# Performance work log

Measured on AMD Instinct MI355X. Metric: run time of the kernel, lower is better.

The kernel has to match this reference:

```python
import jax, jax.numpy as jnp
import numpy as np
import math

EPS = 1.0
N_IT = 10

def _sinkhorn_plan(C, eps, n_it):
    # C: [N, S, Sk] cost matrix; uniform marginals; log-domain Sinkhorn.
    n_rows, n_cols = C.shape[-2], C.shape[-1]
    log_mu = jnp.full(C.shape[:-1], -math.log(n_rows), C.dtype)
    log_nu = jnp.full(C.shape[:-2] + (n_cols,), -math.log(n_cols), C.dtype)

    def M(u, v):
        return (-C + u[..., :, None] + v[..., None, :]) / eps

    def body(carry, _):
        u, v = carry
        u = eps * (log_mu - jax.scipy.special.logsumexp(M(u, v), axis=-1)) + u
        v = eps * (log_nu - jax.scipy.special.logsumexp(M(u, v), axis=-2)) + v
        return (u, v), None

    u0 = jnp.zeros(C.shape[:-1], C.dtype)
    v0 = jnp.zeros(C.shape[:-2] + (C.shape[-1],), C.dtype)
    (u, v), _ = jax.lax.scan(body, (u0, v0), None, length=n_it)
    return jnp.exp(M(u, v))  # transport plan pi


def setup_inputs() -> dict:
    key = jax.random.key(0)
    kq, kk, kv = jax.random.split(key, 3)
    B, H, S, D = 2, 8, 1024, 64
    scale = 0.1  # keep exp(QK^T) numerically safe, as the model would via trained weights
    query = jax.random.normal(kq, (B, H, S, D), jnp.float32) * scale
    k_ = jax.random.normal(kk, (B, H, S, D), jnp.float32) * scale
    value = jax.random.normal(kv, (B, H, S, D), jnp.float32)
    return {"query": query, "key": k_, "value": value}


def reference(query, key, value):
    d = query.shape[-1]
    # exp-score attention (note: exp of raw QK^T, then divide by sqrt(d))
    scores = jnp.exp(jnp.einsum('bhqd,bhkd->bhqk', query, key)) / math.sqrt(d)
    B, H, S, Sk = scores.shape
    attn = scores.reshape(B * H, S, Sk)
    pi = _sinkhorn_plan(attn, EPS, N_IT)
    p_attn = (pi * Sk).reshape(B, H, S, Sk)  # row-stochastic doubly-normalized attention
    out = jnp.einsum('bhqk,bhkd->bhqd', p_attn, value)
    return out, p_attn
```

## Files before the change

kernel.cpp:

```cpp
#include <hip/hip_runtime.h>
#include <math.h>

#define NH   16
#define SEQ  1024
#define DIM  64
#define MUV  (1.0f/1024.0f)
#define KSTRIDE 2048

typedef __attribute__((ext_vector_type(8))) short bf16x8;
typedef __attribute__((ext_vector_type(4))) float f32x4;

__device__ __forceinline__ float frcp(float x){ return __builtin_amdgcn_rcpf(x); }
__device__ __forceinline__ float bf2f(unsigned short u){
  union { unsigned int i; float f; } v; v.i = ((unsigned int)u) << 16; return v.f;
}
__device__ __forceinline__ unsigned short f2bf(float f){
  union { float f; unsigned int i; } v; v.f = f;
  return (unsigned short)((v.i + 0x7FFFu + ((v.i >> 16) & 1u)) >> 16);
}

__global__ __launch_bounds__(256) void qk_kernel(const float* __restrict__ Q,
                                                 const float* __restrict__ Kin,
                                                 unsigned short* __restrict__ Kb) {
  __shared__ unsigned short QS[64 * 64];
  __shared__ unsigned short ST[64 * 64];
  __shared__ unsigned short Ob[64 * 64];
  const int h  = blockIdx.y;
  const int r0 = blockIdx.x * 64;
  const int t  = threadIdx.x;
  const int lane = t & 63, w = t >> 6, fr = lane & 15, fq = lane >> 4;
  const float* Qg = Q   + ((size_t)h * SEQ + r0) * DIM;
  const float* Kg = Kin + (size_t)h * SEQ * DIM;

  {
    const int r = t >> 4, c4 = (t & 15) * 4;
#pragma unroll
    for (int q = 0; q < 4; q++){
      const int row = r + 16 * q;
      const float4 v = *(const float4*)(Qg + row * DIM + c4);
      ushort4 u4 = make_ushort4(f2bf(v.x), f2bf(v.y), f2bf(v.z), f2bf(v.w));
      *(ushort4*)((char*)QS + row * 128 + ((c4 * 2) ^ ((row & 7) << 4))) = u4;
    }
  }
  __syncthreads();

  const int qrow = w * 16 + fr;
  const bf16x8 qa0 = *(const bf16x8*)((char*)QS + qrow * 128 + ((fq * 16)      ^ ((qrow & 7) << 4)));
  const bf16x8 qa1 = *(const bf16x8*)((char*)QS + qrow * 128 + ((64 + fq * 16) ^ ((qrow & 7) << 4)));

  for (int cc = 0; cc < 16; cc++){
    __syncthreads();
    {
      const int r = t >> 4, c4 = (t & 15) * 4;
      const float* g = Kg + (size_t)cc * 64 * DIM;
#pragma unroll
      for (int q = 0; q < 4; q++){
        const int row = r + 16 * q;
        const float4 v = *(const float4*)(g + row * DIM + c4);
        ushort4 u4 = make_ushort4(f2bf(v.x), f2bf(v.y), f2bf(v.z), f2bf(v.w));
        *(ushort4*)((char*)ST + row * 128 + ((c4 * 2) ^ ((row & 7) << 4))) = u4;
      }
    }
    __syncthreads();
#pragma unroll
    for (int ct = 0; ct < 4; ct++){
      const int krow = ct * 16 + fr;
      const bf16x8 kb0 = *(const bf16x8*)((char*)ST + krow * 128 + ((fq * 16)      ^ ((krow & 7) << 4)));
      const bf16x8 kb1 = *(const bf16x8*)((char*)ST + krow * 128 + ((64 + fq * 16) ^ ((krow & 7) << 4)));
      f32x4 acc = {0.f, 0.f, 0.f, 0.f};
      acc = __builtin_amdgcn_mfma_f32_16x16x32_bf16(qa0, kb0, acc, 0, 0, 0);
      acc = __builtin_amdgcn_mfma_f32_16x16x32_bf16(qa1, kb1, acc, 0, 0, 0);
#pragma unroll
      for (int r = 0; r < 4; r++){
        const int roww = w * 16 + fq * 4 + r;
        const float kv = __expf(-__expf(acc[r]) * 0.125f);
        Ob[roww * 64 + ct * 16 + fr] = f2bf(kv);
      }
    }
    __syncthreads();
    {
      const int row = t >> 2, c16 = (t & 3) * 16;
      unsigned short* dst = Kb + (size_t)(h * SEQ + r0 + row) * KSTRIDE + cc * 64 + c16;
      *(uint4*)dst       = *(const uint4*)&Ob[row * 64 + c16];
      *(uint4*)(dst + 8) = *(const uint4*)&Ob[row * 64 + c16 + 8];
    }
  }
}

__global__ __launch_bounds__(256, 2) void sink_iter(const unsigned short* __restrict__ Kb,
                                                    const float* __restrict__ cprev,
                                                    float* __restrict__ cnext,
                                                    float* __restrict__ avg,
                                                    int first) {
  __shared__ unsigned short Ksh[32 * 1024];
  __shared__ float bsh[1024];
  __shared__ float ash[32];
  const int h = blockIdx.y, ch = blockIdx.x, r0 = ch * 32, t = threadIdx.x;

  if (first){
    *(float4*)&bsh[t * 4] = make_float4(1.f, 1.f, 1.f, 1.f);
  } else {
    float4 s = make_float4(0, 0, 0, 0);
    const float* cp = cprev + (size_t)h * 32 * 1024 + t * 4;
#pragma unroll 8
    for (int sl = 0; sl < 32; sl++){
      const float4 v = *(const float4*)(cp + (size_t)sl * 1024);
      s.x += v.x; s.y += v.y; s.z += v.z; s.w += v.w;
    }
    *(float4*)&bsh[t * 4] = make_float4(MUV * frcp(s.x), MUV * frcp(s.y),
                                        MUV * frcp(s.z), MUV * frcp(s.w));
  }
  __syncthreads();

  const int row = t >> 3, off8 = t & 7;
  const unsigned short* gk = Kb + (size_t)(h * SEQ + r0 + row) * KSTRIDE;
  float acc = 0.f;
#pragma unroll
  for (int p = 0; p < 16; p++){
    const int idx = (p * 8 + off8) * 8;
    const uint4 g = *(const uint4*)(gk + idx);
    *(uint4*)&Ksh[row * 1024 + idx] = g;
    const float4 b0 = *(const float4*)&bsh[idx];
    const float4 b1 = *(const float4*)&bsh[idx + 4];
    acc += bf2f((unsigned short)(g.x)) * b0.x + bf2f((unsigned short)(g.x >> 16)) * b0.y
         + bf2f((unsigned short)(g.y)) * b0.z + bf2f((unsigned short)(g.y >> 16)) * b0.w
         + bf2f((unsigned short)(g.z)) * b1.x + bf2f((unsigned short)(g.z >> 16)) * b1.y
         + bf2f((unsigned short)(g.w)) * b1.z + bf2f((unsigned short)(g.w >> 16)) * b1.w;
  }
#pragma unroll
  for (int m = 1; m < 8; m <<= 1) acc += __shfl_xor(acc, m);
  if (off8 == 0){
    const float a = MUV * frcp(acc);
    ash[row] = a;
    avg[h * SEQ + r0 + row] = a;
  }
  __syncthreads();

  float4 ca = make_float4(0, 0, 0, 0);
#pragma unroll 8
  for (int i = 0; i < 32; i++){
    const ushort4 k4 = *(const ushort4*)&Ksh[i * 1024 + t * 4];
    const float a = ash[i];
    ca.x += bf2f(k4.x) * a; ca.y += bf2f(k4.y) * a;
    ca.z += bf2f(k4.z) * a; ca.w += bf2f(k4.w) * a;
  }
  *(float4*)(cnext + ((size_t)h * 32 + ch) * 1024 + t * 4) = ca;
}

__global__ __launch_bounds__(256, 2) void pv_kernel(const unsigned short* __restrict__ Kb,
                                                    const float* __restrict__ V,
                                                    const float* __restrict__ cpart,
                                                    const float* __restrict__ avg,
                                                    float* __restrict__ out) {
  __shared__ unsigned short Ksh[16 * 1024];
  __shared__ unsigned short Vsh[256 * 64];
  __shared__ float bsh[1024];
  __shared__ float ash[16];
  const int h = blockIdx.y, ch = blockIdx.x, r0 = ch * 16, t = threadIdx.x;
  const int lane = t & 63, w = t >> 6, fr = lane & 15, fq = lane >> 4;

  {
    float4 s = make_float4(0, 0, 0, 0);
    const float* cp = cpart + (size_t)h * 32 * 1024 + t * 4;
#pragma unroll 8
    for (int sl = 0; sl < 32; sl++){
      const float4 v = *(const float4*)(cp + (size_t)sl * 1024);
      s.x += v.x; s.y += v.y; s.z += v.z; s.w += v.w;
    }
    *(float4*)&bsh[t * 4] = make_float4(MUV * frcp(s.x), MUV * frcp(s.y),
                                        MUV * frcp(s.z), MUV * frcp(s.w));
  }
  if (t < 16) ash[t] = 1024.f * avg[h * SEQ + r0 + t];

  {
#pragma unroll
    for (int s = 0; s < 8; s++){
      const int u = s * 256 + t;
      const int row = u >> 7, uo = u & 127;
      const unsigned short* src = Kb + (size_t)(h * SEQ + r0 + row) * KSTRIDE + uo * 8;
      *(uint4*)((char*)Ksh + row * 2048 + ((uo * 16) ^ ((row & 7) << 4))) = *(const uint4*)src;
    }
  }
  __syncthreads();

  const float ascale = ash[fr];
  f32x4 oacc = {0.f, 0.f, 0.f, 0.f};
  const float* Vg = V + (size_t)h * SEQ * DIM;

  for (int vq = 0; vq < 4; vq++){
    __syncthreads();
    {
#pragma unroll
      for (int p = 0; p < 4; p++){
        const int j = p * 64 + (t >> 2);
        const int piece = t & 3;
        const float* g = Vg + (size_t)(vq * 256 + j) * DIM + piece * 16;
        union { unsigned short u[16]; uint4 q[2]; } pk;
#pragma unroll
        for (int k = 0; k < 4; k++){
          const float4 v = *(const float4*)(g + k * 4);
          pk.u[k*4+0] = f2bf(v.x); pk.u[k*4+1] = f2bf(v.y);
          pk.u[k*4+2] = f2bf(v.z); pk.u[k*4+3] = f2bf(v.w);
        }
        const int sw = (j & 7) << 4;
        *(uint4*)((char*)Vsh + j * 128 + (((piece * 32)      ) ^ sw)) = pk.q[0];
        *(uint4*)((char*)Vsh + j * 128 + (((piece * 32) + 16 ) ^ sw)) = pk.q[1];
      }
    }
    __syncthreads();
#pragma unroll
    for (int vc = 0; vc < 4; vc++){
#pragma unroll
      for (int half = 0; half < 2; half++){
        const int jl = vc * 64 + half * 32;
        const int jg = vq * 256 + jl;
        const int k0 = jg + fq * 8;
        const bf16x8 kx8 = *(const bf16x8*)((char*)Ksh + fr * 2048 + ((k0 * 2) ^ ((fr & 7) << 4)));
        const float4 b0 = *(const float4*)&bsh[k0];
        const float4 b1 = *(const float4*)&bsh[k0 + 4];
        const float bv[8] = {b0.x, b0.y, b0.z, b0.w, b1.x, b1.y, b1.z, b1.w};
        union { unsigned short u[8]; bf16x8 v; } pa;
#pragma unroll
        for (int e = 0; e < 8; e++)
          pa.u[e] = f2bf(ascale * bv[e] * bf2f((unsigned short)kx8[e]));
        union { unsigned int wv[4]; bf16x8 v; } vb;
        const int dcol = (w * 16 + fr) * 2;
#pragma unroll
        for (int e2 = 0; e2 < 4; e2++){
          const int j0 = jl + fq * 8 + e2 * 2;
          const unsigned int lo = *(const unsigned short*)((char*)Vsh + j0 * 128 + (dcol ^ ((j0 & 7) << 4)));
          const unsigned int hi = *(const unsigned short*)((char*)Vsh + (j0 + 1) * 128 + (dcol ^ (((j0 + 1) & 7) << 4)));
          vb.wv[e2] = lo | (hi << 16);
        }
        oacc = __builtin_amdgcn_mfma_f32_16x16x32_bf16(pa.v, vb.v, oacc, 0, 0, 0);
      }
    }
  }

  float* og = out + ((size_t)h * SEQ + r0) * DIM + w * 16 + fr;
#pragma unroll
  for (int r = 0; r < 4; r++)
    og[(size_t)(fq * 4 + r) * DIM] = oacc[r];
}

__global__ __launch_bounds__(256, 2) void pwrite_kernel(const unsigned short* __restrict__ Kb,
                                                        float* __restrict__ Pmat,
                                                        const float* __restrict__ cpart,
                                                        const float* __restrict__ avg) {
  __shared__ unsigned short Ksh[32 * 1024];
  __shared__ float bsh[1024];
  __shared__ float ash[32];
  const int h = blockIdx.y, ch = blockIdx.x, r0 = ch * 32, t = threadIdx.x;

  {
    float4 s = make_float4(0, 0, 0, 0);
    const float* cp = cpart + (size_t)h * 32 * 1024 + t * 4;
#pragma unroll 8
    for (int sl = 0; sl < 32; sl++){
      const float4 v = *(const float4*)(cp + (size_t)sl * 1024);
      s.x += v.x; s.y += v.y; s.z += v.z; s.w += v.w;
    }
    *(float4*)&bsh[t * 4] = make_float4(MUV * frcp(s.x), MUV * frcp(s.y),
                                        MUV * frcp(s.z), MUV * frcp(s.w));
  }
  if (t < 32) ash[t] = 1024.f * avg[h * SEQ + r0 + t];

  const int row = t >> 3, off8 = t & 7;
  const unsigned short* gk = Kb + (size_t)(h * SEQ + r0 + row) * KSTRIDE;
#pragma unroll
  for (int p = 0; p < 16; p++){
    const int idx = (p * 8 + off8) * 8;
    *(uint4*)&Ksh[row * 1024 + idx] = *(const uint4*)(gk + idx);
  }
  __syncthreads();

  const float ar = ash[row];
  float* prow = Pmat + (size_t)(h * SEQ + r0 + row) * SEQ;
#pragma unroll
  for (int p = 0; p < 16; p++){
    const int idx = (p * 8 + off8) * 8;
    const uint4 g = *(const uint4*)&Ksh[row * 1024 + idx];
    const float4 b0 = *(const float4*)&bsh[idx];
    const float4 b1 = *(const float4*)&bsh[idx + 4];
    float4 o0, o1;
    o0.x = ar * b0.x * bf2f((unsigned short)(g.x));
    o0.y = ar * b0.y * bf2f((unsigned short)(g.x >> 16));
    o0.z = ar * b0.z * bf2f((unsigned short)(g.y));
    o0.w = ar * b0.w * bf2f((unsigned short)(g.y >> 16));
    o1.x = ar * b1.x * bf2f((unsigned short)(g.z));
    o1.y = ar * b1.y * bf2f((unsigned short)(g.z >> 16));
    o1.z = ar * b1.z * bf2f((unsigned short)(g.w));
    o1.w = ar * b1.w * bf2f((unsigned short)(g.w >> 16));
    *(float4*)(prow + idx)     = o0;
    *(float4*)(prow + idx + 4) = o1;
  }
}

extern "C" void kernel_launch(void* const* d_in, const int* in_sizes, int n_in,
                              void* d_out, int out_size, void* d_ws, size_t ws_size,
                              hipStream_t stream) {
  (void)in_sizes; (void)n_in; (void)out_size; (void)ws_size;
  const float* Q   = (const float*)d_in[0];
  const float* Kin = (const float*)d_in[1];
  const float* V   = (const float*)d_in[2];
  float* out  = (float*)d_out;
  float* Pmat = out + (size_t)NH * SEQ * DIM;
  unsigned short* Kb = (unsigned short*)Pmat;

  float* ws  = (float*)d_ws;
  float* cp0 = ws;
  float* cp1 = ws + (size_t)NH * 32 * SEQ;
  float* avg = ws + (size_t)2 * NH * 32 * SEQ;

  qk_kernel<<<dim3(16, 16), 256, 0, stream>>>(Q, Kin, Kb);
  for (int it = 0; it < 10; it++){
    const float* cprev = (it & 1) ? cp0 : cp1;
    float*       cnext = (it & 1) ? cp1 : cp0;
    sink_iter<<<dim3(32, 16), 256, 0, stream>>>(Kb, cprev, cnext, avg, it == 0 ? 1 : 0);
  }
  pv_kernel<<<dim3(64, 16), 256, 0, stream>>>(Kb, V, cp1, avg, out);
  pwrite_kernel<<<dim3(32, 16), 256, 0, stream>>>(Kb, Pmat, cp1, avg);
}
```

Before: 274.9 us.

## Recompute Gibbs kernel via MFMA each Sinkhorn iteration instead of storing it

Stops materialising the bf16 kernel matrix exp(-exp(QK)/8) in global memory. Each Sinkhorn iteration now recomputes QK^T with MFMA from bf16 Q/K copies held in the workspace. A new prep kernel converts Q, K and a transposed V to bf16 once. The P-matrix write and the PV product are fused into one final kernel. This swaps about 32MB of kernel-matrix traffic per iteration for extra matrix-core work and two exponentials per element per iteration.

```diff
diff --git a/kernel.cpp b/kernel.cpp
--- a/kernel.cpp
+++ b/kernel.cpp
@@ -5,7 +5,6 @@
 #define SEQ  1024
 #define DIM  64
 #define MUV  (1.0f/1024.0f)
-#define KSTRIDE 2048
 
 typedef __attribute__((ext_vector_type(8))) short bf16x8;
 typedef __attribute__((ext_vector_type(4))) float f32x4;
@@ -19,83 +18,65 @@
   return (unsigned short)((v.i + 0x7FFFu + ((v.i >> 16) & 1u)) >> 16);
 }
 
-__global__ __launch_bounds__(256) void qk_kernel(const float* __restrict__ Q,
-                                                 const float* __restrict__ Kin,
-                                                 unsigned short* __restrict__ Kb) {
-  __shared__ unsigned short QS[64 * 64];
-  __shared__ unsigned short ST[64 * 64];
-  __shared__ unsigned short Ob[64 * 64];
-  const int h  = blockIdx.y;
-  const int r0 = blockIdx.x * 64;
-  const int t  = threadIdx.x;
-  const int lane = t & 63, w = t >> 6, fr = lane & 15, fq = lane >> 4;
-  const float* Qg = Q   + ((size_t)h * SEQ + r0) * DIM;
-  const float* Kg = Kin + (size_t)h * SEQ * DIM;
-
-  {
-    const int r = t >> 4, c4 = (t & 15) * 4;
-#pragma unroll
-    for (int q = 0; q < 4; q++){
-      const int row = r + 16 * q;
-      const float4 v = *(const float4*)(Qg + row * DIM + c4);
-      ushort4 u4 = make_ushort4(f2bf(v.x), f2bf(v.y), f2bf(v.z), f2bf(v.w));
-      *(ushort4*)((char*)QS + row * 128 + ((c4 * 2) ^ ((row & 7) << 4))) = u4;
-    }
-  }
-  __syncthreads();
-
-  const int qrow = w * 16 + fr;
-  const bf16x8 qa0 = *(const bf16x8*)((char*)QS + qrow * 128 + ((fq * 16)      ^ ((qrow & 7) << 4)));
-  const bf16x8 qa1 = *(const bf16x8*)((char*)QS + qrow * 128 + ((64 + fq * 16) ^ ((qrow & 7) << 4)));
-
-  for (int cc = 0; cc < 16; cc++){
+__global__ __launch_bounds__(256) void prep_kernel(const float* __restrict__ Q,
+                                                   const float* __restrict__ K,
+                                                   const float* __restrict__ V,
+                                                   unsigned short* __restrict__ Qbf,
+                                                   unsigned short* __restrict__ Kbf,
+                                                   unsigned short* __restrict__ Vt) {
+  __shared__ float Vsh[64][68];
+  const int h = blockIdx.y, ck = blockIdx.x, t = threadIdx.x;
+  const int r = t >> 2, cp = (t & 3) * 16;
+  const size_t gbase = ((size_t)h * SEQ + ck * 64 + r) * DIM + cp;
+  {
+    union { unsigned short u[16]; uint4 q[2]; } pk;
+#pragma unroll
+    for (int k = 0; k < 4; k++){
+      const float4 v = *(const float4*)(Q + gbase + k * 4);
+      pk.u[k*4+0]=f2bf(v.x); pk.u[k*4+1]=f2bf(v.y); pk.u[k*4+2]=f2bf(v.z); pk.u[k*4+3]=f2bf(v.w);
+    }
+    *(uint4*)(Qbf + gbase) = pk.q[0];
+    *(uint4*)(Qbf + gbase + 8) = pk.q[1];
+  }
+  {
+    union { unsigned short u[16]; uint4 q[2]; } pk;
+#pragma unroll
+    for (int k = 0; k < 4; k++){
+      const float4 v = *(const float4*)(K + gbase + k * 4);
+      pk.u[k*4+0]=f2bf(v.x); pk.u[k*4+1]=f2bf(v.y); pk.u[k*4+2]=f2bf(v.z); pk.u[k*4+3]=f2bf(v.w);
+    }
+    *(uint4*)(Kbf + gbase) = pk.q[0];
+    *(uint4*)(Kbf + gbase + 8) = pk.q[1];
+  }
+  {
+#pragma unroll
+    for (int k = 0; k < 4; k++)
+      *(float4*)&Vsh[r][cp + k * 4] = *(const float4*)(V + gbase + k * 4);
     __syncthreads();
-    {
-      const int r = t >> 4, c4 = (t & 15) * 4;
-      const float* g = Kg + (size_t)cc * 64 * DIM;
-#pragma unroll
-      for (int q = 0; q < 4; q++){
-        const int row = r + 16 * q;
-        const float4 v = *(const float4*)(g + row * DIM + c4);
-        ushort4 u4 = make_ushort4(f2bf(v.x), f2bf(v.y), f2bf(v.z), f2bf(v.w));
-        *(ushort4*)((char*)ST + row * 128 + ((c4 * 2) ^ ((row & 7) << 4))) = u4;
-      }
-    }
-    __syncthreads();
-#pragma unroll
-    for (int ct = 0; ct < 4; ct++){
-      const int krow = ct * 16 + fr;
-      const bf16x8 kb0 = *(const bf16x8*)((char*)ST + krow * 128 + ((fq * 16)      ^ ((krow & 7) << 4)));
-      const bf16x8 kb1 = *(const bf16x8*)((char*)ST + krow * 128 + ((64 + fq * 16) ^ ((krow & 7) << 4)));
-      f32x4 acc = {0.f, 0.f, 0.f, 0.f};
-      acc = __builtin_amdgcn_mfma_f32_16x16x32_bf16(qa0, kb0, acc, 0, 0, 0);
-      acc = __builtin_amdgcn_mfma_f32_16x16x32_bf16(qa1, kb1, acc, 0, 0, 0);
-#pragma unroll
-      for (int r = 0; r < 4; r++){
-        const int roww = w * 16 + fq * 4 + r;
-        const float kv = __expf(-__expf(acc[r]) * 0.125f);
-        Ob[roww * 64 + ct * 16 + fr] = f2bf(kv);
-      }
-    }
-    __syncthreads();
-    {
-      const int row = t >> 2, c16 = (t & 3) * 16;
-      unsigned short* dst = Kb + (size_t)(h * SEQ + r0 + row) * KSTRIDE + cc * 64 + c16;
-      *(uint4*)dst       = *(const uint4*)&Ob[row * 64 + c16];
-      *(uint4*)(dst + 8) = *(const uint4*)&Ob[row * 64 + c16 + 8];
-    }
-  }
-}
-
-__global__ __launch_bounds__(256, 2) void sink_iter(const unsigned short* __restrict__ Kb,
-                                                    const float* __restrict__ cprev,
-                                                    float* __restrict__ cnext,
-                                                    float* __restrict__ avg,
-                                                    int first) {
+    const int dd = t >> 2, jp = (t & 3) * 16;
+    union { unsigned short u[16]; uint4 q[2]; } pk;
+#pragma unroll
+    for (int k = 0; k < 16; k++) pk.u[k] = f2bf(Vsh[jp + k][dd]);
+    unsigned short* dst = Vt + ((size_t)h * DIM + dd) * SEQ + ck * 64 + jp;
+    *(uint4*)dst       = pk.q[0];
+    *(uint4*)(dst + 8) = pk.q[1];
+  }
+}
+
+__global__ __launch_bounds__(256, 2)
+void sink_rc(const unsigned short* __restrict__ Qbf,
+             const unsigned short* __restrict__ Kbf,
+             const float* __restrict__ cprev,
+             float* __restrict__ cnext,
+             float* __restrict__ avg,
+             int first)
+{
   __shared__ unsigned short Ksh[32 * 1024];
   __shared__ float bsh[1024];
+  __shared__ float rsum[4][32];
   __shared__ float ash[32];
   const int h = blockIdx.y, ch = blockIdx.x, r0 = ch * 32, t = threadIdx.x;
+  const int lane = t & 63, w = t >> 6, fr = lane & 15, fq = lane >> 4;
 
   if (first){
     *(float4*)&bsh[t * 4] = make_float4(1.f, 1.f, 1.f, 1.f);
@@ -112,34 +93,68 @@
   }
   __syncthreads();
 
-  const int row = t >> 3, off8 = t & 7;
-  const unsigned short* gk = Kb + (size_t)(h * SEQ + r0 + row) * KSTRIDE;
-  float acc = 0.f;
-#pragma unroll
-  for (int p = 0; p < 16; p++){
-    const int idx = (p * 8 + off8) * 8;
-    const uint4 g = *(const uint4*)(gk + idx);
-    *(uint4*)&Ksh[row * 1024 + idx] = g;
-    const float4 b0 = *(const float4*)&bsh[idx];
-    const float4 b1 = *(const float4*)&bsh[idx + 4];
-    acc += bf2f((unsigned short)(g.x)) * b0.x + bf2f((unsigned short)(g.x >> 16)) * b0.y
-         + bf2f((unsigned short)(g.y)) * b0.z + bf2f((unsigned short)(g.y >> 16)) * b0.w
-         + bf2f((unsigned short)(g.z)) * b1.x + bf2f((unsigned short)(g.z >> 16)) * b1.y
-         + bf2f((unsigned short)(g.w)) * b1.z + bf2f((unsigned short)(g.w >> 16)) * b1.w;
-  }
-#pragma unroll
-  for (int m = 1; m < 8; m <<= 1) acc += __shfl_xor(acc, m);
-  if (off8 == 0){
-    const float a = MUV * frcp(acc);
-    ash[row] = a;
-    avg[h * SEQ + r0 + row] = a;
+  const unsigned short* qp = Qbf + ((size_t)h * SEQ + r0 + fr) * DIM + fq * 8;
+  const bf16x8 qa00 = *(const bf16x8*)qp;
+  const bf16x8 qa01 = *(const bf16x8*)(qp + 32);
+  const bf16x8 qa10 = *(const bf16x8*)(qp + 16 * DIM);
+  const bf16x8 qa11 = *(const bf16x8*)(qp + 16 * DIM + 32);
+
+  float rp[8] = {0.f,0.f,0.f,0.f,0.f,0.f,0.f,0.f};
+
+#pragma unroll 2
+  for (int cc = 0; cc < 16; cc++){
+    const int c0 = cc * 64 + w * 16;
+    const unsigned short* kp = Kbf + ((size_t)h * SEQ + c0 + fr) * DIM + fq * 8;
+    const bf16x8 kb0 = *(const bf16x8*)kp;
+    const bf16x8 kb1 = *(const bf16x8*)(kp + 32);
+    f32x4 a0 = {0.f,0.f,0.f,0.f}, a1 = {0.f,0.f,0.f,0.f};
+    a0 = __builtin_amdgcn_mfma_f32_16x16x32_bf16(qa00, kb0, a0, 0, 0, 0);
+    a0 = __builtin_amdgcn_mfma_f32_16x16x32_bf16(qa01, kb1, a0, 0, 0, 0);
+    a1 = __builtin_amdgcn_mfma_f32_16x16x32_bf16(qa10, kb0, a1, 0, 0, 0);
+    a1 = __builtin_amdgcn_mfma_f32_16x16x32_bf16(qa11, kb1, a1, 0, 0, 0);
+    const float bcol = bsh[c0 + fr];
+    const int col2 = (c0 + fr) * 2;
+#pragma unroll
+    for (int r = 0; r < 4; r++){
+      const int row0 = fq * 4 + r;
+      const float kv0 = __expf(-0.125f * __expf(a0[r]));
+      const unsigned short ku0 = f2bf(kv0);
+      *(unsigned short*)((char*)Ksh + row0 * 2048 + (col2 ^ ((row0 & 7) << 4))) = ku0;
+      rp[r] += bf2f(ku0) * bcol;
+      const int row1 = 16 + fq * 4 + r;
+      const float kv1 = __expf(-0.125f * __expf(a1[r]));
+      const unsigned short ku1 = f2bf(kv1);
+      *(unsigned short*)((char*)Ksh + row1 * 2048 + (col2 ^ ((row1 & 7) << 4))) = ku1;
+      rp[4 + r] += bf2f(ku1) * bcol;
+    }
+  }
+
+#pragma unroll
+  for (int m = 1; m <= 8; m <<= 1){
+#pragma unroll
+    for (int i = 0; i < 8; i++) rp[i] += __shfl_xor(rp[i], m);
+  }
+  if (fr == 0){
+#pragma unroll
+    for (int r = 0; r < 4; r++){
+      rsum[w][fq * 4 + r]      = rp[r];
+      rsum[w][16 + fq * 4 + r] = rp[4 + r];
+    }
   }
   __syncthreads();
+  if (t < 32){
+    const float rs = rsum[0][t] + rsum[1][t] + rsum[2][t] + rsum[3][t];
+    const float a = MUV * frcp(rs);
+    ash[t] = a;
+    avg[h * SEQ + r0 + t] = a;
+  }
+  __syncthreads();
 
   float4 ca = make_float4(0, 0, 0, 0);
+  const int bo = t * 8;
 #pragma unroll 8
   for (int i = 0; i < 32; i++){
-    const ushort4 k4 = *(const ushort4*)&Ksh[i * 1024 + t * 4];
+    const ushort4 k4 = *(const ushort4*)((char*)Ksh + i * 2048 + (bo ^ ((i & 7) << 4)));
     const float a = ash[i];
     ca.x += bf2f(k4.x) * a; ca.y += bf2f(k4.y) * a;
     ca.z += bf2f(k4.z) * a; ca.w += bf2f(k4.w) * a;
@@ -147,16 +162,19 @@
   *(float4*)(cnext + ((size_t)h * 32 + ch) * 1024 + t * 4) = ca;
 }
 
-__global__ __launch_bounds__(256, 2) void pv_kernel(const unsigned short* __restrict__ Kb,
-                                                    const float* __restrict__ V,
-                                                    const float* __restrict__ cpart,
-                                                    const float* __restrict__ avg,
-                                                    float* __restrict__ out) {
-  __shared__ unsigned short Ksh[16 * 1024];
-  __shared__ unsigned short Vsh[256 * 64];
+__global__ __launch_bounds__(256, 2)
+void final_rc(const unsigned short* __restrict__ Qbf,
+              const unsigned short* __restrict__ Kbf,
+              const unsigned short* __restrict__ Vt,
+              const float* __restrict__ cpart,
+              const float* __restrict__ avg,
+              float* __restrict__ Pmat,
+              float* __restrict__ out)
+{
+  __shared__ unsigned short Ksh[32 * 1024];
   __shared__ float bsh[1024];
-  __shared__ float ash[16];
-  const int h = blockIdx.y, ch = blockIdx.x, r0 = ch * 16, t = threadIdx.x;
+  __shared__ float ash[32];
+  const int h = blockIdx.y, ch = blockIdx.x, r0 = ch * 32, t = threadIdx.x;
   const int lane = t & 63, w = t >> 6, fr = lane & 15, fq = lane >> 4;
 
   {
@@ -170,154 +188,121 @@
     *(float4*)&bsh[t * 4] = make_float4(MUV * frcp(s.x), MUV * frcp(s.y),
                                         MUV * frcp(s.z), MUV * frcp(s.w));
   }
-  if (t < 16) ash[t] = 1024.f * avg[h * SEQ + r0 + t];
-
-  {
-#pragma unroll
-    for (int s = 0; s < 8; s++){
-      const int u = s * 256 + t;
-      const int row = u >> 7, uo = u & 127;
-      const unsigned short* src = Kb + (size_t)(h * SEQ + r0 + row) * KSTRIDE + uo * 8;
-      *(uint4*)((char*)Ksh + row * 2048 + ((uo * 16) ^ ((row & 7) << 4))) = *(const uint4*)src;
+  if (t < 32) ash[t] = 1024.f * avg[h * SEQ + r0 + t];
+
+  const unsigned short* qp = Qbf + ((size_t)h * SEQ + r0 + fr) * DIM + fq * 8;
+  const bf16x8 qa00 = *(const bf16x8*)qp;
+  const bf16x8 qa01 = *(const bf16x8*)(qp + 32);
+  const bf16x8 qa10 = *(const bf16x8*)(qp + 16 * DIM);
+  const bf16x8 qa11 = *(const bf16x8*)(qp + 16 * DIM + 32);
+
+#pragma unroll 2
+  for (int cc = 0; cc < 16; cc++){
+    const int c0 = cc * 64 + w * 16;
+    const unsigned short* kp = Kbf + ((size_t)h * SEQ + c0 + fr) * DIM + fq * 8;
+    const bf16x8 kb0 = *(const bf16x8*)kp;
+    const bf16x8 kb1 = *(const bf16x8*)(kp + 32);
+    f32x4 a0 = {0.f,0.f,0.f,0.f}, a1 = {0.f,0.f,0.f,0.f};
+    a0 = __builtin_amdgcn_mfma_f32_16x16x32_bf16(qa00, kb0, a0, 0, 0, 0);
+    a0 = __builtin_amdgcn_mfma_f32_16x16x32_bf16(qa01, kb1, a0, 0, 0, 0);
+    a1 = __builtin_amdgcn_mfma_f32_16x16x32_bf16(qa10, kb0, a1, 0, 0, 0);
+    a1 = __builtin_amdgcn_mfma_f32_16x16x32_bf16(qa11, kb1, a1, 0, 0, 0);
+    const int col2 = (c0 + fr) * 2;
+#pragma unroll
+    for (int r = 0; r < 4; r++){
+      const int row0 = fq * 4 + r;
+      *(unsigned short*)((char*)Ksh + row0 * 2048 + (col2 ^ ((row0 & 7) << 4))) =
+          f2bf(__expf(-0.125f * __expf(a0[r])));
+      const int row1 = 16 + fq * 4 + r;
+      *(unsigned short*)((char*)Ksh + row1 * 2048 + (col2 ^ ((row1 & 7) << 4))) =
+          f2bf(__expf(-0.125f * __expf(a1[r])));
     }
   }
   __syncthreads();
 
-  const float ascale = ash[fr];
-  f32x4 oacc = {0.f, 0.f, 0.f, 0.f};
-  const float* Vg = V + (size_t)h * SEQ * DIM;
-
-  for (int vq = 0; vq < 4; vq++){
-    __syncthreads();
-    {
-#pragma unroll
-      for (int p = 0; p < 4; p++){
-        const int j = p * 64 + (t >> 2);
-        const int piece = t & 3;
-        const float* g = Vg + (size_t)(vq * 256 + j) * DIM + piece * 16;
-        union { unsigned short u[16]; uint4 q[2]; } pk;
-#pragma unroll
-        for (int k = 0; k < 4; k++){
-          const float4 v = *(const float4*)(g + k * 4);
-          pk.u[k*4+0] = f2bf(v.x); pk.u[k*4+1] = f2bf(v.y);
-          pk.u[k*4+2] = f2bf(v.z); pk.u[k*4+3] = f2bf(v.w);
-        }
-        const int sw = (j & 7) << 4;
-        *(uint4*)((char*)Vsh + j * 128 + (((piece * 32)      ) ^ sw)) = pk.q[0];
-        *(uint4*)((char*)Vsh + j * 128 + (((piece * 32) + 16 ) ^ sw)) = pk.q[1];
-      }
-    }
-    __syncthreads();
-#pragma unroll
-    for (int vc = 0; vc < 4; vc++){
-#pragma unroll
-      for (int half = 0; half < 2; half++){
-        const int jl = vc * 64 + half * 32;
-        const int jg = vq * 256 + jl;
-        const int k0 = jg + fq * 8;
-        const bf16x8 kx8 = *(const bf16x8*)((char*)Ksh + fr * 2048 + ((k0 * 2) ^ ((fr & 7) << 4)));
-        const float4 b0 = *(const float4*)&bsh[k0];
-        const float4 b1 = *(const float4*)&bsh[k0 + 4];
-        const float bv[8] = {b0.x, b0.y, b0.z, b0.w, b1.x, b1.y, b1.z, b1.w};
-        union { unsigned short u[8]; bf16x8 v; } pa;
-#pragma unroll
-        for (int e = 0; e < 8; e++)
-          pa.u[e] = f2bf(ascale * bv[e] * bf2f((unsigned short)kx8[e]));
-        union { unsigned int wv[4]; bf16x8 v; } vb;
-        const int dcol = (w * 16 + fr) * 2;
-#pragma unroll
-        for (int e2 = 0; e2 < 4; e2++){
-          const int j0 = jl + fq * 8 + e2 * 2;
-          const unsigned int lo = *(const unsigned short*)((char*)Vsh + j0 * 128 + (dcol ^ ((j0 & 7) << 4)));
-          const unsigned int hi = *(const unsigned short*)((char*)Vsh + (j0 + 1) * 128 + (dcol ^ (((j0 + 1) & 7) << 4)));
-          vb.wv[e2] = lo | (hi << 16);
-        }
-        oacc = __builtin_amdgcn_mfma_f32_16x16x32_bf16(pa.v, vb.v, oacc, 0, 0, 0);
-      }
-    }
+  {
+    const int prow = t >> 3, pc = t & 7;
+    const float ar = ash[prow];
+    const int swp = (prow & 7) << 4;
+    float* pg = Pmat + ((size_t)h * SEQ + r0 + prow) * SEQ;
+#pragma unroll
+    for (int p16 = 0; p16 < 16; p16++){
+      const int colb = (p16 * 8 + pc) * 8;
+      const uint4 kq = *(const uint4*)((char*)Ksh + prow * 2048 + ((colb * 2) ^ swp));
+      const float4 b0 = *(const float4*)&bsh[colb];
+      const float4 b1 = *(const float4*)&bsh[colb + 4];
+      float4 o0, o1;
+      o0.x = ar * b0.x * bf2f((unsigned short)(kq.x));
+      o0.y = ar * b0.y * bf2f((unsigned short)(kq.x >> 16));
+      o0.z = ar * b0.z * bf2f((unsigned short)(kq.y));
+      o0.w = ar * b0.w * bf2f((unsigned short)(kq.y >> 16));
+      o1.x = ar * b1.x * bf2f((unsigned short)(kq.z));
+      o1.y = ar * b1.y * bf2f((unsigned short)(kq.z >> 16));
+      o1.z = ar * b1.z * bf2f((unsigned short)(kq.w));
+      o1.w = ar * b1.w * bf2f((unsigned short)(kq.w >> 16));
+      *(float4*)(pg + colb)     = o0;
+      *(float4*)(pg + colb + 4) = o1;
+    }
+  }
+
+  f32x4 o0 = {0.f,0.f,0.f,0.f}, o1 = {0.f,0.f,0.f,0.f};
+  const float ar0 = ash[fr];
+  const float ar1 = ash[16 + fr];
+  const int sw0 = (fr & 7) << 4;
+  const char* kr0 = (const char*)Ksh + fr * 2048;
+  const char* kr1 = (const char*)Ksh + (16 + fr) * 2048;
+  const unsigned short* vp = Vt + ((size_t)h * DIM + w * 16 + fr) * SEQ;
+#pragma unroll 2
+  for (int jc = 0; jc < 32; jc++){
+    const int jb = jc * 32 + fq * 8;
+    const bf16x8 vb = *(const bf16x8*)(vp + jb);
+    const float4 b0 = *(const float4*)&bsh[jb];
+    const float4 b1 = *(const float4*)&bsh[jb + 4];
+    const float bv[8] = {b0.x, b0.y, b0.z, b0.w, b1.x, b1.y, b1.z, b1.w};
+    const bf16x8 k0 = *(const bf16x8*)(kr0 + ((jb * 2) ^ sw0));
+    const bf16x8 k1 = *(const bf16x8*)(kr1 + ((jb * 2) ^ sw0));
+    union { unsigned short u[8]; bf16x8 v; } pa0, pa1;
+#pragma unroll
+    for (int e = 0; e < 8; e++){
+      pa0.u[e] = f2bf(ar0 * bv[e] * bf2f((unsigned short)k0[e]));
+      pa1.u[e] = f2bf(ar1 * bv[e] * bf2f((unsigned short)k1[e]));
+    }
+    o0 = __builtin_amdgcn_mfma_f32_16x16x32_bf16(pa0.v, vb, o0, 0, 0, 0);
+    o1 = __builtin_amdgcn_mfma_f32_16x16x32_bf16(pa1.v, vb, o1, 0, 0, 0);
   }
 
   float* og = out + ((size_t)h * SEQ + r0) * DIM + w * 16 + fr;
 #pragma unroll
   for (int r = 0; r < 4; r++)
-    og[(size_t)(fq * 4 + r) * DIM] = oacc[r];
-}
-
-__global__ __launch_bounds__(256, 2) void pwrite_kernel(const unsigned short* __restrict__ Kb,
-                                                        float* __restrict__ Pmat,
-                                                        const float* __restrict__ cpart,
-                                                        const float* __restrict__ avg) {
-  __shared__ unsigned short Ksh[32 * 1024];
-  __shared__ float bsh[1024];
-  __shared__ float ash[32];
-  const int h = blockIdx.y, ch = blockIdx.x, r0 = ch * 32, t = threadIdx.x;
-
-  {
-    float4 s = make_float4(0, 0, 0, 0);
-    const float* cp = cpart + (size_t)h * 32 * 1024 + t * 4;
-#pragma unroll 8
-    for (int sl = 0; sl < 32; sl++){
-      const float4 v = *(const float4*)(cp + (size_t)sl * 1024);
-      s.x += v.x; s.y += v.y; s.z += v.z; s.w += v.w;
-    }
-    *(float4*)&bsh[t * 4] = make_float4(MUV * frcp(s.x), MUV * frcp(s.y),
-                                        MUV * frcp(s.z), MUV * frcp(s.w));
-  }
-  if (t < 32) ash[t] = 1024.f * avg[h * SEQ + r0 + t];
-
-  const int row = t >> 3, off8 = t & 7;
-  const unsigned short* gk = Kb + (size_t)(h * SEQ + r0 + row) * KSTRIDE;
-#pragma unroll
-  for (int p = 0; p < 16; p++){
-    const int idx = (p * 8 + off8) * 8;
-    *(uint4*)&Ksh[row * 1024 + idx] = *(const uint4*)(gk + idx);
-  }
-  __syncthreads();
-
-  const float ar = ash[row];
-  float* prow = Pmat + (size_t)(h * SEQ + r0 + row) * SEQ;
-#pragma unroll
-  for (int p = 0; p < 16; p++){
-    const int idx = (p * 8 + off8) * 8;
-    const uint4 g = *(const uint4*)&Ksh[row * 1024 + idx];
-    const float4 b0 = *(const float4*)&bsh[idx];
-    const float4 b1 = *(const float4*)&bsh[idx + 4];
-    float4 o0, o1;
-    o0.x = ar * b0.x * bf2f((unsigned short)(g.x));
-    o0.y = ar * b0.y * bf2f((unsigned short)(g.x >> 16));
-    o0.z = ar * b0.z * bf2f((unsigned short)(g.y));
-    o0.w = ar * b0.w * bf2f((unsigned short)(g.y >> 16));
-    o1.x = ar * b1.x * bf2f((unsigned short)(g.z));
-    o1.y = ar * b1.y * bf2f((unsigned short)(g.z >> 16));
-    o1.z = ar * b1.z * bf2f((unsigned short)(g.w));
-    o1.w = ar * b1.w * bf2f((unsigned short)(g.w >> 16));
-    *(float4*)(prow + idx)     = o0;
-    *(float4*)(prow + idx + 4) = o1;
-  }
+    og[(size_t)(fq * 4 + r) * DIM] = o0[r];
+  float* og1 = og + (size_t)16 * DIM;
+#pragma unroll
+  for (int r = 0; r < 4; r++)
+    og1[(size_t)(fq * 4 + r) * DIM] = o1[r];
 }
 
 extern "C" void kernel_launch(void* const* d_in, const int* in_sizes, int n_in,
                               void* d_out, int out_size, void* d_ws, size_t ws_size,
                               hipStream_t stream) {
   (void)in_sizes; (void)n_in; (void)out_size; (void)ws_size;
-  const float* Q   = (const float*)d_in[0];
-  const float* Kin = (const float*)d_in[1];
-  const float* V   = (const float*)d_in[2];
+  const float* Q = (const float*)d_in[0];
+  const float* K = (const float*)d_in[1];
+  const float* V = (const float*)d_in[2];
   float* out  = (float*)d_out;
   float* Pmat = out + (size_t)NH * SEQ * DIM;
-  unsigned short* Kb = (unsigned short*)Pmat;
-
-  float* ws  = (float*)d_ws;
-  float* cp0 = ws;
-  float* cp1 = ws + (size_t)NH * 32 * SEQ;
-  float* avg = ws + (size_t)2 * NH * 32 * SEQ;
-
-  qk_kernel<<<dim3(16, 16), 256, 0, stream>>>(Q, Kin, Kb);
+
+  unsigned short* Qbf = (unsigned short*)d_ws;
+  unsigned short* Kbf = Qbf + (size_t)NH * SEQ * DIM;
+  unsigned short* Vt  = Kbf + (size_t)NH * SEQ * DIM;
+  float* cp0 = (float*)(Vt + (size_t)NH * SEQ * DIM);
+  float* cp1 = cp0 + (size_t)NH * 32 * SEQ;
+  float* avg = cp1 + (size_t)NH * 32 * SEQ;
+
+  prep_kernel<<<dim3(16, 16), 256, 0, stream>>>(Q, K, V, Qbf, Kbf, Vt);
   for (int it = 0; it < 10; it++){
     const float* cprev = (it & 1) ? cp0 : cp1;
     float*       cnext = (it & 1) ? cp1 : cp0;
-    sink_iter<<<dim3(32, 16), 256, 0, stream>>>(Kb, cprev, cnext, avg, it == 0 ? 1 : 0);
-  }
-  pv_kernel<<<dim3(64, 16), 256, 0, stream>>>(Kb, V, cp1, avg, out);
-  pwrite_kernel<<<dim3(32, 16), 256, 0, stream>>>(Kb, Pmat, cp1, avg);
-}
+    sink_rc<<<dim3(32, 16), 256, 0, stream>>>(Qbf, Kbf, cprev, cnext, avg, it == 0 ? 1 : 0);
+  }
+  final_rc<<<dim3(32, 16), 256, 0, stream>>>(Qbf, Kbf, Vt, cp1, avg, Pmat, out);
+}
```

Result: no change. 271.5 us (-1.2%).
